# Kernel tuning notes

Measured on AMD Instinct MI355X. Metric: run time of the kernel, lower is better.

## Reference

```python
import jax, jax.numpy as jnp
import numpy as np

EPS = 1e-5
K = 32

def _bn(x, g, b, m, v):
    # eval-mode BatchNorm over channel (last) axis
    return (x - m) * jax.lax.rsqrt(v + EPS) * g + b

def _attn_pool(x, sw, sb, mw, mb):
    # x: [B, N, C]; scores softmax over N
    s = jax.nn.softmax(jnp.einsum('bnc,oc->bno', x, sw) + sb, axis=1)  # [B,N,1]
    pooled = jnp.sum(s * x, axis=1)  # [B,C]
    return pooled @ mw.T + mb

def setup_inputs() -> dict:
    key = jax.random.key(0)
    ks = jax.random.split(key, 16)
    B, N, G = 8, 8192, 512
    d = {}
    d['xyz'] = jax.random.normal(ks[0], (B, N, 3), jnp.float32)
    d['center_idx'] = jax.random.randint(ks[1], (B, G), 0, N, jnp.int64)
    s = lambda k, shp, f: (jax.random.normal(k, shp, jnp.float32) * f)
    d['w1'] = s(ks[2], (128, 10), 0.3); d['b1'] = jnp.zeros((128,))
    d['g1'] = jnp.ones((128,)); d['be1'] = jnp.zeros((128,))
    d['m1'] = jnp.zeros((128,)); d['v1'] = jnp.ones((128,))
    d['w2'] = s(ks[3], (256, 128), 0.08); d['b2'] = jnp.zeros((256,))
    d['ap1_sw'] = s(ks[4], (1, 256), 0.06); d['ap1_sb'] = jnp.zeros((1,))
    d['ap1_mw'] = s(ks[5], (256, 256), 0.06); d['ap1_mb'] = jnp.zeros((256,))
    d['w3'] = s(ks[6], (512, 512), 0.04); d['b3'] = jnp.zeros((512,))
    d['g2'] = jnp.ones((512,)); d['be2'] = jnp.zeros((512,))
    d['m2'] = jnp.zeros((512,)); d['v2'] = jnp.ones((512,))
    d['w4'] = s(ks[7], (512, 512), 0.04); d['b4'] = jnp.zeros((512,))
    d['ap2_sw'] = s(ks[8], (1, 512), 0.04); d['ap2_sb'] = jnp.zeros((1,))
    d['ap2_mw'] = s(ks[9], (512, 512), 0.04); d['ap2_mb'] = jnp.zeros((512,))
    return d

def reference(xyz, center_idx, w1, b1, g1, be1, m1, v1, w2, b2,
              ap1_sw, ap1_sb, ap1_mw, ap1_mb, w3, b3, g2, be2, m2, v2,
              w4, b4, ap2_sw, ap2_sb, ap2_mw, ap2_mb):
    B, N, _ = xyz.shape
    G = center_idx.shape[1]
    # center sampling (replaces misc.random_sample with explicit indices)
    center = jnp.take_along_axis(xyz, center_idx[..., None], axis=1)  # [B,G,3]
    # knn: squared pairwise distances, top-k smallest
    d2 = (jnp.sum(center**2, -1)[:, :, None] + jnp.sum(xyz**2, -1)[:, None, :]
          - 2.0 * jnp.einsum('bgc,bnc->bgn', center, xyz))  # [B,G,N]
    _, idx = jax.lax.top_k(-d2, K)  # [B,G,K]
    neighborhood = jax.vmap(lambda pts, i: pts[i])(xyz, idx)  # [B,G,K,3]
    xyz_tile = jnp.broadcast_to(center[:, :, None, :], (B, G, K, 3))
    rel = xyz_tile - neighborhood
    rdist = jnp.sqrt(jnp.sum(rel**2, -1, keepdims=True))
    feat = jnp.concatenate([rdist, rel, xyz_tile, neighborhood], -1)  # [B,G,K,10]
    x = feat.reshape(B * G, K, 10)
    # first_conv: 1x1 convs == per-point linear
    x = jax.nn.relu(_bn(jnp.einsum('bnc,oc->bno', x, w1) + b1, g1, be1, m1, v1))
    x = jnp.einsum('bnc,oc->bno', x, w2) + b2  # [BG,K,256]
    fg = _attn_pool(x, ap1_sw, ap1_sb, ap1_mw, ap1_mb)  # [BG,256]
    x = jnp.concatenate([jnp.broadcast_to(fg[:, None, :], x.shape), x], -1)  # [BG,K,512]
    x = jax.nn.relu(_bn(jnp.einsum('bnc,oc->bno', x, w3) + b3, g2, be2, m2, v2))
    x = jnp.einsum('bnc,oc->bno', x, w4) + b4  # [BG,K,512]
    fg2 = _attn_pool(x, ap2_sw, ap2_sb, ap2_mw, ap2_mb)  # [BG,512]
    return center, fg2.reshape(B, G, 512)
```

## Files before the change

kernel.cpp:

```cpp
#include <hip/hip_runtime.h>
#include <math.h>

#define EPSV 1e-5f

typedef __attribute__((ext_vector_type(8))) short bf16x8;
typedef __attribute__((ext_vector_type(4))) float f32x4;

#define MFMA16(a, b, c) __builtin_amdgcn_mfma_f32_16x16x32_bf16(a, b, c, 0, 0, 0)

__device__ __forceinline__ short f2bf(float x) {
    unsigned u = __float_as_uint(x);
    unsigned r = (u + 0x7fffu + ((u >> 16) & 1u)) >> 16;
    return (short)r;
}
__device__ __forceinline__ float bf2f(short h) {
    return __uint_as_float(((unsigned)(unsigned short)h) << 16);
}
__device__ __forceinline__ void bsplit(float x, short& h, short& l) {
    h = f2bf(x);
    l = f2bf(x - bf2f(h));
}
__device__ __forceinline__ unsigned pack2(short a, short b) {
    return ((unsigned)(unsigned short)a) | (((unsigned)(unsigned short)b) << 16);
}

#define KCAP 2048
__global__ __launch_bounds__(256) void prep_knn(
    const float* __restrict__ xyz, const int* __restrict__ cidx,
    int* __restrict__ knn_idx, float* __restrict__ out_center,
    const float* __restrict__ w1, const float* __restrict__ b1,
    const float* __restrict__ w2, const float* __restrict__ w3,
    const float* __restrict__ mw1, const float* __restrict__ mw2,
    const float* __restrict__ w4, const float* __restrict__ b4,
    const float* __restrict__ sw2, const float* __restrict__ sb2,
    const float* __restrict__ mb2, const float* __restrict__ mb1,
    const float* __restrict__ b3,
    const float* __restrict__ g1, const float* __restrict__ be1,
    const float* __restrict__ m1, const float* __restrict__ v1,
    const float* __restrict__ g2, const float* __restrict__ be2,
    const float* __restrict__ m2, const float* __restrict__ v2,
    short* __restrict__ w1fh, short* __restrict__ w2fh, short* __restrict__ w3fh,
    short* __restrict__ Pfh, short* __restrict__ MTfh,
    float* __restrict__ sc1, float* __restrict__ shb1,
    float* __restrict__ sc2, float* __restrict__ sh2,
    float* __restrict__ u, float* __restrict__ bb, float* __restrict__ ub,
    float* __restrict__ bc3)
{
    __shared__ __align__(16) char shm[12416];
    int B = blockIdx.x, t = threadIdx.x;
    int lane = t & 63, w = t >> 6;

    if (B < 4096) {
        unsigned* cu = (unsigned*)shm;
        unsigned short* cix = (unsigned short*)(shm + 8192);
        unsigned* Tws = (unsigned*)(shm + 12288);
        unsigned* cntS = (unsigned*)(shm + 12304);
        int g = B, b = g >> 9;
        const float* xb = xyz + (size_t)b * 8192 * 3;
        int ci = cidx[g];
        float cx = xb[ci * 3 + 0], cy = xb[ci * 3 + 1], cz = xb[ci * 3 + 2];
        float c2 = cx * cx + cy * cy + cz * cz;
        if (t < 3) out_center[g * 3 + t] = xb[ci * 3 + t];
        if (t == 0) *cntS = 0;

        const float4* p4 = (const float4*)xb + (size_t)t * 24;
        unsigned ue[32];
        unsigned vmin = 0xffffffffu;
        #pragma unroll
        for (int ii = 0; ii < 8; ++ii) {
            float4 v0 = p4[ii * 3 + 0];
            float4 v1 = p4[ii * 3 + 1];
            float4 v2 = p4[ii * 3 + 2];
            float px[4], py[4], pz[4];
            px[0] = v0.x; py[0] = v0.y; pz[0] = v0.z;
            px[1] = v0.w; py[1] = v1.x; pz[1] = v1.y;
            px[2] = v1.z; py[2] = v1.w; pz[2] = v2.x;
            px[3] = v2.y; py[3] = v2.z; pz[3] = v2.w;
            #pragma unroll
            for (int m = 0; m < 4; ++m) {
                float dx = px[m], dy = py[m], dz = pz[m];
                float n2 = dx * dx + dy * dy + dz * dz;
                float d = c2 + n2 - 2.f * (cx * dx + cy * dy + cz * dz);
                unsigned uu = __float_as_uint(d);
                uu = (uu & 0x80000000u) ? ~uu : (uu | 0x80000000u);
                ue[ii * 4 + m] = uu;
                vmin = min(vmin, uu);
            }
        }
        unsigned v = vmin;
        #pragma unroll
        for (int k = 2; k <= 64; k <<= 1) {
            #pragma unroll
            for (int jj = k >> 1; jj > 0; jj >>= 1) {
                unsigned o = __shfl_xor(v, jj);
                bool dir_asc = ((lane & k) == 0) || (k == 64);
                bool lower = (lane & jj) == 0;
                bool take_min = (lower == dir_asc);
                unsigned mn = min(v, o), mx = max(v, o);
                v = take_min ? mn : mx;
            }
        }
        unsigned Tw = __shfl(v, 31);
        if (lane == 0) Tws[w] = Tw;
        __syncthreads();
        unsigned T = min(min(Tws[0], Tws[1]), min(Tws[2], Tws[3]));
        #pragma unroll
        for (int i = 0; i < 32; ++i) {
            if (ue[i] <= T) {
                unsigned pos = atomicAdd(cntS, 1u);
                if (pos < KCAP) {
                    cu[pos] = ue[i];
                    cix[pos] = (unsigned short)(t * 32 + i);
                }
            }
        }
        __syncthreads();
        int C = (int)min(*cntS, (unsigned)KCAP);
        for (int cc = t; cc < C; cc += 256) {
            unsigned uc = cu[cc];
            unsigned short icd = cix[cc];
            int rank = 0;
            for (int j = 0; j < C; ++j) {
                unsigned uj = cu[j];
                rank += (uj < uc) || (uj == uc && cix[j] < icd);
            }
            if (rank < 32) knn_idx[g * 32 + rank] = (int)icd;
        }
        return;
    }

    if (B < 4352) {
        float* col = (float*)shm;
        int c = B - 4096;
        col[t] = mw1[t * 256 + c];
        __syncthreads();
        int ks = c >> 5, qq = (c >> 3) & 3, jj = c & 7;
        for (int oo = t; oo < 512; oo += 256) {
            float acc = 0.f;
            for (int d = 0; d < 256; ++d) acc += col[d] * w3[oo * 512 + d];
            int ct = oo >> 4;
            size_t idx = ((size_t)(ct * 8 + ks) * 64 + qq * 16 + (oo & 15)) * 8 + jj;
            Pfh[idx] = f2bf(acc);
        }
        return;
    }

    if (B < 4864) {
        float* row = (float*)shm;
        int qq = B - 4352;
        row[t] = mw2[(size_t)qq * 512 + t];
        row[t + 256] = mw2[(size_t)qq * 512 + t + 256];
        __syncthreads();
        float a0 = 0.f, a1 = 0.f;
        for (int o = 0; o < 512; ++o) {
            float m = row[o];
            a0 += m * w4[o * 512 + t];
            a1 += m * w4[o * 512 + t + 256];
        }
        int ct = qq >> 4, nl = qq & 15;
        {
            int k = t;
            size_t i0 = (((size_t)(ct * 16 + (k >> 5))) << 9)
                      | ((((k >> 3) & 3) * 16 + nl) << 3) | (k & 7);
            MTfh[i0] = f2bf(a0);
        }
        {
            int k = t + 256;
            size_t i1 = (((size_t)(ct * 16 + (k >> 5))) << 9)
                      | ((((k >> 3) & 3) * 16 + nl) << 3) | (k & 7);
            MTfh[i1] = f2bf(a1);
        }
        return;
    }

    if (B < 4992) {
        int tid = (B - 4864) * 256 + t;
        {
            int i = tid;
            int j = i & 7, ln = (i >> 3) & 63, rest = i >> 9;
            int ks = rest & 3, ct = rest >> 2;
            int o = ct * 16 + (ln & 15);
            int k = ks * 32 + (ln >> 4) * 8 + j;
            w2fh[i] = f2bf(w2[o * 128 + k]);
        }
        #pragma unroll
        for (int s = 0; s < 4; ++s) {
            int i = tid + s * 32768;
            int j = i & 7, ln = (i >> 3) & 63, rest = i >> 9;
            int ks = rest & 7, ct = rest >> 3;
            int o = ct * 16 + (ln & 15);
            int c = 256 + ks * 32 + (ln >> 4) * 8 + j;
            w3fh[i] = f2bf(w3[o * 512 + c]);
        }
        return;
    }

    if (B < 5056) {
        float* b4s = (float*)shm;
        float* red = (float*)(shm + 2048);
        b4s[t] = b4[t];
        b4s[t + 256] = b4[t + 256];
        __syncthreads();
        int q0 = (B - 4992) * 8;
        for (int i = 0; i < 8; ++i) {
            int q = q0 + i;
            float part = mw2[(size_t)q * 512 + t] * b4s[t]
                       + mw2[(size_t)q * 512 + 256 + t] * b4s[256 + t];
            #pragma unroll
            for (int off = 32; off > 0; off >>= 1) part += __shfl_down(part, off);
            if (lane == 0) red[w] = part;
            __syncthreads();
            if (t == 0) bb[q] = mb2[q] + red[0] + red[1] + red[2] + red[3];
            __syncthreads();
        }
        return;
    }

    if (B < 5120) {
        float* mb1s = (float*)shm;
        float* red = (float*)(shm + 1024);
        mb1s[t] = mb1[t];
        __syncthreads();
        int o0 = (B - 5056) * 8;
        for (int i = 0; i < 8; ++i) {
            int o = o0 + i;
            float part = w3[(size_t)o * 512 + t] * mb1s[t];
            #pragma unroll
            for (int off = 32; off > 0; off >>= 1) part += __shfl_down(part, off);
            if (lane == 0) red[w] = part;
            __syncthreads();
            if (t == 0) bc3[o] = b3[o] + red[0] + red[1] + red[2] + red[3];
            __syncthreads();
        }
        return;
    }

    if (B < 5122) {
        int c = (B - 5120) * 256 + t;
        float acc = 0.f;
        for (int o = 0; o < 512; ++o) acc += sw2[o] * w4[o * 512 + c];
        u[c] = acc;
        return;
    }

    if (t < 128) {
        float s = g1[t] * rsqrtf(v1[t] + EPSV);
        float sh = be1[t] - m1[t] * s;
        sc1[t] = s;
        shb1[t] = b1[t] * s + sh;
    }
    {
        float s = g2[t] * rsqrtf(v2[t] + EPSV);
        sc2[t] = s; sh2[t] = be2[t] - m2[t] * s;
        s = g2[t + 256] * rsqrtf(v2[t + 256] + EPSV);
        sc2[t + 256] = s; sh2[t + 256] = be2[t + 256] - m2[t + 256] * s;
    }
    #pragma unroll
    for (int s = 0; s < 16; ++s) {
        int i = t + s * 256;
        int j = i & 7, ln = (i >> 3) & 63, ct = i >> 9;
        int o = ct * 16 + (ln & 15);
        int k = (ln >> 4) * 8 + j;
        w1fh[i] = (k < 10) ? f2bf(w1[o * 10 + k]) : (short)0;
    }
    if (t < 64) {
        float part = 0.f;
        #pragma unroll
        for (int i = 0; i < 8; ++i) part += sw2[t * 8 + i] * b4[t * 8 + i];
        #pragma unroll
        for (int off = 32; off > 0; off >>= 1) part += __shfl_down(part, off);
        if (t == 0) ub[0] = sb2[0] + part;
    }
}

__global__ __launch_bounds__(512) void mlp_kernel(
    const float* __restrict__ xyz, const int* __restrict__ cidx,
    const int* __restrict__ knn_idx,
    const short* __restrict__ w1fh,
    const float* __restrict__ sc1, const float* __restrict__ shb1,
    const short* __restrict__ w2fh,
    const float* __restrict__ b2,
    const float* __restrict__ sw1, const float* __restrict__ sb1,
    const short* __restrict__ Pfh, const float* __restrict__ bc3,
    const short* __restrict__ w3fh,
    const float* __restrict__ sc2, const float* __restrict__ sh2,
    const float* __restrict__ u, const float* __restrict__ ubp,
    short* __restrict__ yh)
{
    __shared__ __align__(16) char smem[70656];
    short* x1 = (short*)smem;
    short* x2 = (short*)smem;
    short* feat = (short*)(smem + 32768);
    short* poolA = (short*)(smem + 65536);
    float* scs = (float*)(smem + 69632);
    float* sms = (float*)(smem + 70144);

    int gb = blockIdx.x * 4;
    int bq = gb >> 9;
    int t = threadIdx.x;
    int lane = t & 63, wv = t >> 6, q = lane >> 4, r = lane & 15;
    const float* xb = xyz + (size_t)bq * 8192 * 3;

    if (t < 128) {
        int gg = t >> 5;
        int ci = cidx[gb + gg];
        float cxx = xb[ci * 3 + 0], cyy = xb[ci * 3 + 1], czz = xb[ci * 3 + 2];
        int n = knn_idx[(gb + gg) * 32 + (t & 31)];
        float nx = xb[n * 3 + 0], ny = xb[n * 3 + 1], nz = xb[n * 3 + 2];
        float rx = cxx - nx, ry = cyy - ny, rz = czz - nz;
        float rd = sqrtf(rx * rx + ry * ry + rz * rz);
        float f[10];
        f[0] = rd; f[1] = rx; f[2] = ry; f[3] = rz;
        f[4] = cxx; f[5] = cyy; f[6] = czz;
        f[7] = nx; f[8] = ny; f[9] = nz;
        unsigned* fr = (unsigned*)(feat + t * 40);
        short h0, l0, h1, l1;
        #pragma unroll
        for (int c = 0; c < 10; c += 2) {
            bsplit(f[c], h0, l0);
            bsplit(f[c + 1], h1, l1);
            fr[c >> 1] = pack2(h0, h1);
            fr[8 + (c >> 1)] = pack2(l0, l1);
        }
        fr[5] = 0; fr[6] = 0; fr[7] = 0;
        fr[13] = 0; fr[14] = 0; fr[15] = 0;
    }
    if (t < 128) scs[t] = sb1[0];
    __syncthreads();

    {
        f32x4 acc1[8];
        #pragma unroll
        for (int rt = 0; rt < 8; ++rt) acc1[rt] = (f32x4){0.f, 0.f, 0.f, 0.f};
        bf16x8 bw = *(const bf16x8*)(w1fh + ((size_t)wv * 64 + lane) * 8);
        bf16x8 zerov = (bf16x8){0, 0, 0, 0, 0, 0, 0, 0};
        #pragma unroll
        for (int rt = 0; rt < 8; ++rt) {
            int row = rt * 16 + r;
            bf16x8 ah = zerov, al = zerov;
            if (q < 2) {
                ah = *(const bf16x8*)(feat + row * 40 + q * 8);
                al = *(const bf16x8*)(feat + row * 40 + 16 + q * 8);
            }
            acc1[rt] = MFMA16(al, bw, acc1[rt]);
            acc1[rt] = MFMA16(ah, bw, acc1[rt]);
        }
        int o = wv * 16 + r;
        float s1v = sc1[o], sbv = shb1[o];
        #pragma unroll
        for (int rt = 0; rt < 8; ++rt)
            #pragma unroll
            for (int j = 0; j < 4; ++j) {
                int row = rt * 16 + q * 4 + j;
                float vv = fmaxf(acc1[rt][j] * s1v + sbv, 0.f);
                x1[row * 128 + (o ^ ((row & 7) << 3))] = f2bf(vv);
            }
    }
    __syncthreads();

    f32x4 acc2[8][2];
    #pragma unroll
    for (int rt = 0; rt < 8; ++rt)
        #pragma unroll
        for (int ctl = 0; ctl < 2; ++ctl) {
            float bv = b2[(wv * 2 + ctl) * 16 + r];
            acc2[rt][ctl] = (f32x4){bv, bv, bv, bv};
        }
    #pragma unroll
    for (int ks = 0; ks < 4; ++ks) {
        bf16x8 af[8];
        #pragma unroll
        for (int rt = 0; rt < 8; ++rt) {
            int row = rt * 16 + r;
            int kk = ks * 32 + q * 8;
            af[rt] = *(const bf16x8*)(x1 + row * 128 + (kk ^ ((row & 7) << 3)));
        }
        #pragma unroll
        for (int ctl = 0; ctl < 2; ++ctl) {
            int ct = wv * 2 + ctl;
            size_t woff = ((size_t)(ct * 4 + ks) * 64 + lane) * 8;
            bf16x8 bh = *(const bf16x8*)(w2fh + woff);
            #pragma unroll
            for (int rt = 0; rt < 8; ++rt)
                acc2[rt][ctl] = MFMA16(af[rt], bh, acc2[rt][ctl]);
        }
    }
    {
        float sw1v[2];
        #pragma unroll
        for (int ctl = 0; ctl < 2; ++ctl) sw1v[ctl] = sw1[(wv * 2 + ctl) * 16 + r];
        #pragma unroll
        for (int rt = 0; rt < 8; ++rt)
            #pragma unroll
            for (int j = 0; j < 4; ++j) {
                float s = sw1v[0] * acc2[rt][0][j] + sw1v[1] * acc2[rt][1][j];
                s += __shfl_xor(s, 1); s += __shfl_xor(s, 2);
                s += __shfl_xor(s, 4); s += __shfl_xor(s, 8);
                if (r == 0) atomicAdd(&scs[rt * 16 + q * 4 + j], s);
            }
    }
    __syncthreads();

    if (wv < 4 && lane < 32) {
        float s = scs[wv * 32 + lane];
        float mx = s;
        mx = fmaxf(mx, __shfl_xor(mx, 16));
        mx = fmaxf(mx, __shfl_xor(mx, 8));
        mx = fmaxf(mx, __shfl_xor(mx, 4));
        mx = fmaxf(mx, __shfl_xor(mx, 2));
        mx = fmaxf(mx, __shfl_xor(mx, 1));
        float e = expf(s - mx);
        float sum = e;
        sum += __shfl_xor(sum, 16);
        sum += __shfl_xor(sum, 8);
        sum += __shfl_xor(sum, 4);
        sum += __shfl_xor(sum, 2);
        sum += __shfl_xor(sum, 1);
        sms[wv * 32 + lane] = e / sum;
    }
    #pragma unroll
    for (int rt = 0; rt < 8; ++rt)
        #pragma unroll
        for (int ctl = 0; ctl < 2; ++ctl) {
            int ch = (wv * 2 + ctl) * 16 + r;
            #pragma unroll
            for (int j = 0; j < 4; ++j) {
                int row = rt * 16 + q * 4 + j;
                x2[row * 256 + (ch ^ ((row & 7) << 3))] = f2bf(acc2[rt][ctl][j]);
            }
        }
    __syncthreads();

    {
        #pragma unroll
        for (int ctl = 0; ctl < 2; ++ctl)
            #pragma unroll
            for (int gg = 0; gg < 4; ++gg) {
                float p = 0.f;
                #pragma unroll
                for (int rr = 0; rr < 2; ++rr) {
                    int rt = gg * 2 + rr;
                    #pragma unroll
                    for (int j = 0; j < 4; ++j)
                        p += sms[rt * 16 + q * 4 + j] * acc2[rt][ctl][j];
                }
                p += __shfl_xor(p, 16);
                p += __shfl_xor(p, 32);
                if (q == 0) {
                    int ch = (wv * 2 + ctl) * 16 + r;
                    short h, l; bsplit(p, h, l);
                    poolA[gg * 256 + (ch ^ (gg << 3))] = h;
                    poolA[(gg + 4) * 256 + (ch ^ ((gg + 4) << 3))] = l;
                }
            }
        if (t < 128) scs[t] = ubp[0];
    }
    __syncthreads();

    float fgv[4][4];
    float bc3v[4];
    {
        f32x4 accP[4];
        #pragma unroll
        for (int ctl = 0; ctl < 4; ++ctl) accP[ctl] = (f32x4){0.f, 0.f, 0.f, 0.f};
        #pragma unroll
        for (int ks = 0; ks < 8; ++ks) {
            int kk = ks * 32 + q * 8;
            bf16x8 pa;
            if (r < 8) pa = *(const bf16x8*)(poolA + r * 256 + (kk ^ (r << 3)));
            else pa = (bf16x8){0, 0, 0, 0, 0, 0, 0, 0};
            #pragma unroll
            for (int ctl = 0; ctl < 4; ++ctl) {
                size_t woff = ((size_t)((wv * 4 + ctl) * 8 + ks) * 64 + lane) * 8;
                bf16x8 ph = *(const bf16x8*)(Pfh + woff);
                accP[ctl] = MFMA16(pa, ph, accP[ctl]);
            }
        }
        #pragma unroll
        for (int ctl = 0; ctl < 4; ++ctl) {
            bc3v[ctl] = bc3[(wv * 4 + ctl) * 16 + r];
            #pragma unroll
            for (int j = 0; j < 4; ++j) {
                float x = accP[ctl][j];
                x += __shfl_xor(x, 16);
                x += __shfl_xor(x, 32);
                fgv[ctl][j] = x;
            }
        }
    }

    f32x4 acc3[8][4];
    #pragma unroll
    for (int rt = 0; rt < 8; ++rt) {
        int gg = rt >> 1;
        #pragma unroll
        for (int ctl = 0; ctl < 4; ++ctl) {
            float fp = fgv[ctl][gg] + bc3v[ctl];
            acc3[rt][ctl] = (f32x4){fp, fp, fp, fp};
        }
    }
    #pragma unroll
    for (int ks = 0; ks < 8; ++ks) {
        bf16x8 af[8];
        #pragma unroll
        for (int rt = 0; rt < 8; ++rt) {
            int row = rt * 16 + r;
            int kk = ks * 32 + q * 8;
            af[rt] = *(const bf16x8*)(x2 + row * 256 + (kk ^ ((row & 7) << 3)));
        }
        #pragma unroll
        for (int ctl = 0; ctl < 4; ++ctl) {
            int ct = wv * 4 + ctl;
            size_t woff = ((size_t)(ct * 8 + ks) * 64 + lane) * 8;
            bf16x8 bh = *(const bf16x8*)(w3fh + woff);
            #pragma unroll
            for (int rt = 0; rt < 8; ++rt)
                acc3[rt][ctl] = MFMA16(af[rt], bh, acc3[rt][ctl]);
        }
    }
    float uv[4];
    {
        #pragma unroll
        for (int ctl = 0; ctl < 4; ++ctl) {
            int ch = (wv * 4 + ctl) * 16 + r;
            float s = sc2[ch], sh = sh2[ch];
            uv[ctl] = u[ch];
            #pragma unroll
            for (int rt = 0; rt < 8; ++rt)
                #pragma unroll
                for (int j = 0; j < 4; ++j)
                    acc3[rt][ctl][j] = fmaxf(acc3[rt][ctl][j] * s + sh, 0.f);
        }
        #pragma unroll
        for (int rt = 0; rt < 8; ++rt)
            #pragma unroll
            for (int j = 0; j < 4; ++j) {
                float s = uv[0] * acc3[rt][0][j] + uv[1] * acc3[rt][1][j]
                        + uv[2] * acc3[rt][2][j] + uv[3] * acc3[rt][3][j];
                s += __shfl_xor(s, 1); s += __shfl_xor(s, 2);
                s += __shfl_xor(s, 4); s += __shfl_xor(s, 8);
                if (r == 0) atomicAdd(&scs[rt * 16 + q * 4 + j], s);
            }
    }
    __syncthreads();

    if (wv < 4 && lane < 32) {
        float s = scs[wv * 32 + lane];
        float mx = s;
        mx = fmaxf(mx, __shfl_xor(mx, 16));
        mx = fmaxf(mx, __shfl_xor(mx, 8));
        mx = fmaxf(mx, __shfl_xor(mx, 4));
        mx = fmaxf(mx, __shfl_xor(mx, 2));
        mx = fmaxf(mx, __shfl_xor(mx, 1));
        float e = expf(s - mx);
        float sum = e;
        sum += __shfl_xor(sum, 16);
        sum += __shfl_xor(sum, 8);
        sum += __shfl_xor(sum, 4);
        sum += __shfl_xor(sum, 2);
        sum += __shfl_xor(sum, 1);
        sms[wv * 32 + lane] = e / sum;
    }
    __syncthreads();

    {
        #pragma unroll
        for (int ctl = 0; ctl < 4; ++ctl)
            #pragma unroll
            for (int gg = 0; gg < 4; ++gg) {
                float p = 0.f;
                #pragma unroll
                for (int rr = 0; rr < 2; ++rr) {
                    int rt = gg * 2 + rr;
                    #pragma unroll
                    for (int j = 0; j < 4; ++j)
                        p += sms[rt * 16 + q * 4 + j] * acc3[rt][ctl][j];
                }
                p += __shfl_xor(p, 16);
                p += __shfl_xor(p, 32);
                if (q == 0) {
                    int grow = gb + gg;
                    int ch = (wv * 4 + ctl) * 16 + r;
                    yh[(size_t)grow * 512 + ch] = f2bf(p);
                }
            }
    }
}

__global__ __launch_bounds__(256) void fg2_kernel(
    const short* __restrict__ yh,
    const short* __restrict__ MTfh,
    const float* __restrict__ bb, float* __restrict__ out_fg2)
{
    int gbase = blockIdx.x * 16;
    int t = threadIdx.x;
    int lane = t & 63, wv = t >> 6, q = lane >> 4, r = lane & 15;
    f32x4 acc[8];
    #pragma unroll
    for (int ctl = 0; ctl < 8; ++ctl) {
        float bv = bb[(wv * 8 + ctl) * 16 + r];
        acc[ctl] = (f32x4){bv, bv, bv, bv};
    }
    #pragma unroll
    for (int ks = 0; ks < 16; ++ks) {
        bf16x8 af = *(const bf16x8*)(yh + (size_t)(gbase + r) * 512 + ks * 32 + q * 8);
        #pragma unroll
        for (int ctl = 0; ctl < 8; ++ctl) {
            int ct = wv * 8 + ctl;
            size_t woff = ((size_t)(ct * 16 + ks) * 64 + lane) * 8;
            bf16x8 bh = *(const bf16x8*)(MTfh + woff);
            acc[ctl] = MFMA16(af, bh, acc[ctl]);
        }
    }
    #pragma unroll
    for (int ctl = 0; ctl < 8; ++ctl) {
        int ch = (wv * 8 + ctl) * 16 + r;
        #pragma unroll
        for (int j = 0; j < 4; ++j) {
            int grow = gbase + q * 4 + j;
            out_fg2[(size_t)grow * 512 + ch] = acc[ctl][j];
        }
    }
}

extern "C" void kernel_launch(void* const* d_in, const int* in_sizes, int n_in,
                              void* d_out, int out_size, void* d_ws, size_t ws_size,
                              hipStream_t stream) {
    const float* xyz  = (const float*)d_in[0];
    const int*   cidx = (const int*)d_in[1];
    const float* w1   = (const float*)d_in[2];
    const float* b1   = (const float*)d_in[3];
    const float* g1   = (const float*)d_in[4];
    const float* be1  = (const float*)d_in[5];
    const float* m1   = (const float*)d_in[6];
    const float* v1   = (const float*)d_in[7];
    const float* w2   = (const float*)d_in[8];
    const float* b2   = (const float*)d_in[9];
    const float* sw1  = (const float*)d_in[10];
    const float* sb1  = (const float*)d_in[11];
    const float* mw1  = (const float*)d_in[12];
    const float* mb1  = (const float*)d_in[13];
    const float* w3   = (const float*)d_in[14];
    const float* b3   = (const float*)d_in[15];
    const float* g2   = (const float*)d_in[16];
    const float* be2  = (const float*)d_in[17];
    const float* m2   = (const float*)d_in[18];
    const float* v2   = (const float*)d_in[19];
    const float* w4   = (const float*)d_in[20];
    const float* b4   = (const float*)d_in[21];
    const float* sw2  = (const float*)d_in[22];
    const float* sb2  = (const float*)d_in[23];
    const float* mw2  = (const float*)d_in[24];
    const float* mb2  = (const float*)d_in[25];

    float* out = (float*)d_out;
    char* ws = (char*)d_ws;
    int*   knn_idx = (int*)(ws + 0);
    short* w2fh = (short*)(ws + 524288);
    short* w3fh = (short*)(ws + 655360);
    short* Pfh  = (short*)(ws + 1179648);
    short* w1fh = (short*)(ws + 1441792);
    float* bc3  = (float*)(ws + 1703936);
    float* sc1  = (float*)(ws + 1705984);
    float* shb1 = (float*)(ws + 1706496);
    float* sc2  = (float*)(ws + 1707008);
    float* sh2  = (float*)(ws + 1709056);
    float* u    = (float*)(ws + 1711104);
    float* bb   = (float*)(ws + 1713152);
    float* ub   = (float*)(ws + 1715200);
    short* MTfh = (short*)(ws + 1715456);
    short* yh   = (short*)(ws + 2764032);

    prep_knn<<<5123, 256, 0, stream>>>(xyz, cidx, knn_idx, out,
                                       w1, b1, w2, w3, mw1, mw2, w4, b4, sw2, sb2,
                                       mb2, mb1, b3,
                                       g1, be1, m1, v1, g2, be2, m2, v2,
                                       w1fh, w2fh, w3fh, Pfh, MTfh,
                                       sc1, shb1, sc2, sh2, u, bb, ub, bc3);
    mlp_kernel<<<1024, 512, 0, stream>>>(xyz, cidx, knn_idx,
                                         w1fh, sc1, shb1, w2fh, b2,
                                         sw1, sb1, Pfh, bc3, w3fh,
                                         sc2, sh2, u, ub, yh);
    fg2_kernel<<<256, 256, 0, stream>>>(yh, MTfh, bb, out + 12288);
}
```

Measured before the change: 333.7 us.

## Interleave output channels in MFMA weight layouts to enable packed bf16 stores

```diff
diff --git a/kernel.cpp b/kernel.cpp
--- a/kernel.cpp
+++ b/kernel.cpp
@@ -22,6 +22,11 @@
 }
 __device__ __forceinline__ unsigned pack2(short a, short b) {
     return ((unsigned)(unsigned short)a) | (((unsigned)(unsigned short)b) << 16);
+}
+__device__ __forceinline__ unsigned cvtpk(float lo, float hi) {
+    unsigned d;
+    asm("v_cvt_pk_bf16_f32 %0, %1, %2" : "=v"(d) : "v"(lo), "v"(hi));
+    return d;
 }
 
 #define KCAP 2048
@@ -138,8 +143,9 @@
         for (int oo = t; oo < 512; oo += 256) {
             float acc = 0.f;
             for (int d = 0; d < 256; ++d) acc += col[d] * w3[oo * 512 + d];
-            int ct = oo >> 4;
-            size_t idx = ((size_t)(ct * 8 + ks) * 64 + qq * 16 + (oo & 15)) * 8 + jj;
+            int ct = (oo >> 6) * 4 + (oo & 3);
+            int n = (oo >> 2) & 15;
+            size_t idx = ((size_t)(ct * 8 + ks) * 64 + qq * 16 + n) * 8 + jj;
             Pfh[idx] = f2bf(acc);
         }
         return;
@@ -179,7 +185,7 @@
             int i = tid;
             int j = i & 7, ln = (i >> 3) & 63, rest = i >> 9;
             int ks = rest & 3, ct = rest >> 2;
-            int o = ct * 16 + (ln & 15);
+            int o = (ct >> 1) * 32 + 2 * (ln & 15) + (ct & 1);
             int k = ks * 32 + (ln >> 4) * 8 + j;
             w2fh[i] = f2bf(w2[o * 128 + k]);
         }
@@ -188,7 +194,7 @@
             int i = tid + s * 32768;
             int j = i & 7, ln = (i >> 3) & 63, rest = i >> 9;
             int ks = rest & 7, ct = rest >> 3;
-            int o = ct * 16 + (ln & 15);
+            int o = (ct >> 2) * 64 + 4 * (ln & 15) + (ct & 3);
             int c = 256 + ks * 32 + (ln >> 4) * 8 + j;
             w3fh[i] = f2bf(w3[o * 512 + c]);
         }
@@ -358,14 +364,16 @@
     }
     __syncthreads();
 
+    int ch2 = wv * 32 + 2 * r;
     f32x4 acc2[8][2];
-    #pragma unroll
-    for (int rt = 0; rt < 8; ++rt)
-        #pragma unroll
-        for (int ctl = 0; ctl < 2; ++ctl) {
-            float bv = b2[(wv * 2 + ctl) * 16 + r];
-            acc2[rt][ctl] = (f32x4){bv, bv, bv, bv};
-        }
+    {
+        float2 b2v = *(const float2*)(b2 + ch2);
+        #pragma unroll
+        for (int rt = 0; rt < 8; ++rt) {
+            acc2[rt][0] = (f32x4){b2v.x, b2v.x, b2v.x, b2v.x};
+            acc2[rt][1] = (f32x4){b2v.y, b2v.y, b2v.y, b2v.y};
+        }
+    }
     #pragma unroll
     for (int ks = 0; ks < 4; ++ks) {
         bf16x8 af[8];
@@ -386,14 +394,12 @@
         }
     }
     {
-        float sw1v[2];
-        #pragma unroll
-        for (int ctl = 0; ctl < 2; ++ctl) sw1v[ctl] = sw1[(wv * 2 + ctl) * 16 + r];
+        float2 sw1v = *(const float2*)(sw1 + ch2);
         #pragma unroll
         for (int rt = 0; rt < 8; ++rt)
             #pragma unroll
             for (int j = 0; j < 4; ++j) {
-                float s = sw1v[0] * acc2[rt][0][j] + sw1v[1] * acc2[rt][1][j];
+                float s = sw1v.x * acc2[rt][0][j] + sw1v.y * acc2[rt][1][j];
                 s += __shfl_xor(s, 1); s += __shfl_xor(s, 2);
                 s += __shfl_xor(s, 4); s += __shfl_xor(s, 8);
                 if (r == 0) atomicAdd(&scs[rt * 16 + q * 4 + j], s);
@@ -421,21 +427,19 @@
     #pragma unroll
     for (int rt = 0; rt < 8; ++rt)
         #pragma unroll
-        for (int ctl = 0; ctl < 2; ++ctl) {
-            int ch = (wv * 2 + ctl) * 16 + r;
-            #pragma unroll
-            for (int j = 0; j < 4; ++j) {
-                int row = rt * 16 + q * 4 + j;
-                x2[row * 256 + (ch ^ ((row & 7) << 3))] = f2bf(acc2[rt][ctl][j]);
-            }
+        for (int j = 0; j < 4; ++j) {
+            int row = rt * 16 + q * 4 + j;
+            unsigned pw = cvtpk(acc2[rt][0][j], acc2[rt][1][j]);
+            *(unsigned*)(x2 + row * 256 + (ch2 ^ ((row & 7) << 3))) = pw;
         }
     __syncthreads();
 
     {
         #pragma unroll
-        for (int ctl = 0; ctl < 2; ++ctl)
-            #pragma unroll
-            for (int gg = 0; gg < 4; ++gg) {
+        for (int gg = 0; gg < 4; ++gg) {
+            float pp[2];
+            #pragma unroll
+            for (int ctl = 0; ctl < 2; ++ctl) {
                 float p = 0.f;
                 #pragma unroll
                 for (int rr = 0; rr < 2; ++rr) {
@@ -446,19 +450,23 @@
                 }
                 p += __shfl_xor(p, 16);
                 p += __shfl_xor(p, 32);
-                if (q == 0) {
-                    int ch = (wv * 2 + ctl) * 16 + r;
-                    short h, l; bsplit(p, h, l);
-                    poolA[gg * 256 + (ch ^ (gg << 3))] = h;
-                    poolA[(gg + 4) * 256 + (ch ^ ((gg + 4) << 3))] = l;
-                }
-            }
+                pp[ctl] = p;
+            }
+            if (q == 0) {
+                unsigned hw = cvtpk(pp[0], pp[1]);
+                float l0 = pp[0] - bf2f((short)(hw & 0xffff));
+                float l1 = pp[1] - bf2f((short)(hw >> 16));
+                unsigned lw = cvtpk(l0, l1);
+                *(unsigned*)(poolA + gg * 256 + (ch2 ^ (gg << 3))) = hw;
+                *(unsigned*)(poolA + (gg + 4) * 256 + (ch2 ^ ((gg + 4) << 3))) = lw;
+            }
+        }
         if (t < 128) scs[t] = ubp[0];
     }
     __syncthreads();
 
     float fgv[4][4];
-    float bc3v[4];
+    f32x4 bc3v = *(const f32x4*)(bc3 + wv * 64 + 4 * r);
     {
         f32x4 accP[4];
         #pragma unroll
@@ -478,7 +486,6 @@
         }
         #pragma unroll
         for (int ctl = 0; ctl < 4; ++ctl) {
-            bc3v[ctl] = bc3[(wv * 4 + ctl) * 16 + r];
             #pragma unroll
             for (int j = 0; j < 4; ++j) {
                 float x = accP[ctl][j];
@@ -518,13 +525,13 @@
                 acc3[rt][ctl] = MFMA16(af[rt], bh, acc3[rt][ctl]);
         }
     }
-    float uv[4];
-    {
+    {
+        f32x4 sc2v = *(const f32x4*)(sc2 + wv * 64 + 4 * r);
+        f32x4 sh2v = *(const f32x4*)(sh2 + wv * 64 + 4 * r);
+        f32x4 uv4  = *(const f32x4*)(u   + wv * 64 + 4 * r);
         #pragma unroll
         for (int ctl = 0; ctl < 4; ++ctl) {
-            int ch = (wv * 4 + ctl) * 16 + r;
-            float s = sc2[ch], sh = sh2[ch];
-            uv[ctl] = u[ch];
+            float s = sc2v[ctl], sh = sh2v[ctl];
             #pragma unroll
             for (int rt = 0; rt < 8; ++rt)
                 #pragma unroll
@@ -535,8 +542,8 @@
         for (int rt = 0; rt < 8; ++rt)
             #pragma unroll
             for (int j = 0; j < 4; ++j) {
-                float s = uv[0] * acc3[rt][0][j] + uv[1] * acc3[rt][1][j]
-                        + uv[2] * acc3[rt][2][j] + uv[3] * acc3[rt][3][j];
+                float s = uv4[0] * acc3[rt][0][j] + uv4[1] * acc3[rt][1][j]
+                        + uv4[2] * acc3[rt][2][j] + uv4[3] * acc3[rt][3][j];
                 s += __shfl_xor(s, 1); s += __shfl_xor(s, 2);
                 s += __shfl_xor(s, 4); s += __shfl_xor(s, 8);
                 if (r == 0) atomicAdd(&scs[rt * 16 + q * 4 + j], s);
@@ -565,9 +572,10 @@
 
     {
         #pragma unroll
-        for (int ctl = 0; ctl < 4; ++ctl)
-            #pragma unroll
-            for (int gg = 0; gg < 4; ++gg) {
+        for (int gg = 0; gg < 4; ++gg) {
+            float p4v[4];
+            #pragma unroll
+            for (int ctl = 0; ctl < 4; ++ctl) {
                 float p = 0.f;
                 #pragma unroll
                 for (int rr = 0; rr < 2; ++rr) {
@@ -578,12 +586,16 @@
                 }
                 p += __shfl_xor(p, 16);
                 p += __shfl_xor(p, 32);
-                if (q == 0) {
-                    int grow = gb + gg;
-                    int ch = (wv * 4 + ctl) * 16 + r;
-                    yh[(size_t)grow * 512 + ch] = f2bf(p);
-                }
-            }
+                p4v[ctl] = p;
+            }
+            if (q == 0) {
+                int grow = gb + gg;
+                uint2 pk;
+                pk.x = cvtpk(p4v[0], p4v[1]);
+                pk.y = cvtpk(p4v[2], p4v[3]);
+                *(uint2*)(yh + (size_t)grow * 512 + wv * 64 + 4 * r) = pk;
+            }
+        }
     }
 }
 
```

Result: faster. 325.7 us (-2.4%).
